# Performance work log

Hardware: AMD Instinct MI355X
Metric: run time of the kernel (lower is better)

The kernel has to match this reference:

```python
import jax, jax.numpy as jnp
import numpy as np

MARGIN_1 = 1.0
MARGIN_2 = 1.5
ALPHA_1 = 2.4
ALPHA_2 = 2.2
TVAL = 1.0
EPS = 1e-5


def setup_inputs() -> dict:
    key = jax.random.key(0)
    k1, k2, k3 = jax.random.split(key, 3)
    N, D = 4096, 2048
    x = jax.random.normal(k1, (N, D), dtype=jnp.float32)
    targets = jax.random.randint(k2, (N,), 0, 128, dtype=jnp.int32)
    sub = jax.random.randint(k3, (N,), 0, 2, dtype=jnp.int32)
    return {"x": x, "targets": targets, "sub": sub}


def _euclidean_dist(x):
    # pairwise distances of rows, clamped like torch .clamp(min=1e-12).sqrt()
    sq = jnp.sum(x * x, axis=1)  # [N]
    d2 = sq[:, None] + sq[None, :] - 2.0 * (x @ x.T)
    return jnp.sqrt(jnp.maximum(d2, 1e-12))  # [N, N]


def reference(x, targets, sub):
    # L2 normalize rows (norm=True path)
    x = x / jnp.maximum(jnp.linalg.norm(x, axis=1, keepdims=True), 1e-12)
    dist = _euclidean_dist(x)  # [N, N]
    N = dist.shape[0]

    eye = jnp.eye(N, dtype=bool)
    same_id = targets[:, None] == targets[None, :]
    is_pos = same_id & ~eye
    is_neg = ~same_id
    intra = sub[:, None] == sub[None, :]

    m_pos_intra = is_pos & intra
    m_pos_cross = is_pos & ~intra
    m_neg_intra = is_neg & intra
    m_neg_cross = is_neg & ~intra

    def ap_term(mask, margin, alpha):
        vals = jnp.maximum(dist + (margin - alpha), 0.0)
        cnt = jnp.sum(mask, axis=1).astype(dist.dtype)
        return jnp.sum(jnp.where(mask, vals, 0.0), axis=1) / (cnt + EPS)

    def an_term(mask, alpha):
        sel = mask & (dist < alpha)
        diff = alpha - dist  # = (alpha - d); weight = exp(tval * diff)
        w = jnp.where(sel, jnp.exp(TVAL * diff), 0.0)
        num = jnp.sum(jnp.where(sel, diff, 0.0) * w, axis=1)
        den = jnp.sum(w, axis=1) + EPS
        return num / den

    loss_rows = (
        ap_term(m_pos_intra, MARGIN_1, ALPHA_1)
        + ap_term(m_pos_cross, MARGIN_2, ALPHA_2)
        + an_term(m_neg_intra, ALPHA_1)
        + an_term(m_neg_cross, ALPHA_2)
    )
    return jnp.sum(loss_rows) / N
```

## Files before the change

### kernel.cpp

```cpp
#include <hip/hip_runtime.h>
#include <math.h>

#define THREADS 256
#define BM 128
#define QBK 128
#define EPSV 1e-5f
#define C1E 11.023176380641601f
#define C2E 9.025013499434122f
#define FP8_SCALE 256.0f
#define INV_SCALE2 1.52587890625e-5f

typedef float f32x4 __attribute__((ext_vector_type(4)));

__launch_bounds__(THREADS)
__global__ void norm_conv_fp8_kernel(const float* __restrict__ x,
                                     unsigned char* __restrict__ xq, int D) {
    const int row = blockIdx.x;
    const float4* x4 = (const float4*)(x + (size_t)row * D);
    const int tid = threadIdx.x;

    float s = 0.f;
    for (int b = tid * 2; b * 4 < D; b += THREADS * 2) {
        float4 v0 = x4[b];
        float4 v1 = x4[b + 1];
        s += v0.x * v0.x + v0.y * v0.y + v0.z * v0.z + v0.w * v0.w
           + v1.x * v1.x + v1.y * v1.y + v1.z * v1.z + v1.w * v1.w;
    }
#pragma unroll
    for (int off = 32; off > 0; off >>= 1) s += __shfl_down(s, off, 64);
    __shared__ float red[THREADS / 64 + 1];
    if ((tid & 63) == 0) red[tid >> 6] = s;
    __syncthreads();
    if (tid == 0) {
        float tot = 0.f;
#pragma unroll
        for (int w = 0; w < THREADS / 64; ++w) tot += red[w];
        red[THREADS / 64] = FP8_SCALE / fmaxf(sqrtf(tot), 1e-12f);
    }
    __syncthreads();
    const float sc = red[THREADS / 64];

    int2* out = (int2*)(xq + (size_t)row * D);
    for (int b = tid * 2; b * 4 < D; b += THREADS * 2) {
        float4 v0 = x4[b];
        float4 v1 = x4[b + 1];
        int lo = __builtin_amdgcn_cvt_pk_fp8_f32(v0.x * sc, v0.y * sc, 0, 0);
        lo = __builtin_amdgcn_cvt_pk_fp8_f32(v0.z * sc, v0.w * sc, lo, 1);
        int hi = __builtin_amdgcn_cvt_pk_fp8_f32(v1.x * sc, v1.y * sc, 0, 0);
        hi = __builtin_amdgcn_cvt_pk_fp8_f32(v1.z * sc, v1.w * sc, hi, 1);
        int2 o; o.x = lo; o.y = hi;
        out[b >> 1] = o;
    }
}

__global__ void row_inv_norm_kernel(const float* __restrict__ x,
                                    float* __restrict__ inv_norm, int D) {
    const int row = blockIdx.x;
    const float4* x4 = (const float4*)(x + (size_t)row * D);
    const int nf4 = D >> 2;
    float s = 0.f;
    for (int i = threadIdx.x; i < nf4; i += THREADS) {
        float4 v = x4[i];
        s += v.x * v.x + v.y * v.y + v.z * v.z + v.w * v.w;
    }
#pragma unroll
    for (int off = 32; off > 0; off >>= 1) s += __shfl_down(s, off, 64);
    __shared__ float red[THREADS / 64];
    if ((threadIdx.x & 63) == 0) red[threadIdx.x >> 6] = s;
    __syncthreads();
    if (threadIdx.x == 0) {
        float tot = 0.f;
#pragma unroll
        for (int w = 0; w < THREADS / 64; ++w) tot += red[w];
        inv_norm[row] = 1.0f / fmaxf(sqrtf(tot), 1e-12f);
    }
}

#define GLDS16(g, l)                                                          \
    __builtin_amdgcn_global_load_lds(                                         \
        (const __attribute__((address_space(1))) unsigned int*)(g),           \
        (__attribute__((address_space(3))) unsigned int*)(l), 16, 0, 0)

__launch_bounds__(THREADS, 2)
__global__ void gram_fp8_kernel(const unsigned char* __restrict__ xq,
                                const int* __restrict__ targets,
                                const int* __restrict__ sub,
                                float* __restrict__ pr,
                                float* __restrict__ pc,
                                int D) {
    __shared__ unsigned char As[2][BM * QBK];
    __shared__ unsigned char Bs[2][BM * QBK];

    const int tk = blockIdx.x;
    int bx = (int)((sqrtf(8.0f * tk + 1.0f) - 1.0f) * 0.5f);
    while ((bx + 1) * (bx + 2) / 2 <= tk) ++bx;
    while (bx * (bx + 1) / 2 > tk) --bx;
    const int by = tk - bx * (bx + 1) / 2;

    const int tid = threadIdx.x;
    const int w = tid >> 6;
    const int lane = tid & 63;
    const int wm = w & 1;
    const int wn = w >> 1;
    const int quad = lane >> 4;
    const int cl = lane & 15;

    const int rowA0 = by * BM;
    const int colB0 = bx * BM;
    const unsigned char* Abase = xq + (size_t)rowA0 * D;
    const unsigned char* Bbase = xq + (size_t)colB0 * D;

    const unsigned char* sA[4];
    const unsigned char* sB[4];
    int dof[4];
#pragma unroll
    for (int l = 0; l < 4; ++l) {
        const int c = l * 256 + tid;
        const int r = c >> 3, q = (c & 7) ^ ((c >> 3) & 7);
        sA[l] = Abase + (size_t)r * D + q * 16;
        sB[l] = Bbase + (size_t)r * D + q * 16;
        dof[l] = (l * 256 + w * 64) * 16;
    }

    f32x4 accv[4][4];
#pragma unroll
    for (int i = 0; i < 4; ++i)
#pragma unroll
        for (int j = 0; j < 4; ++j) accv[i][j] = (f32x4)(0.f);

    int aoff[4][4], boff[4][4];
#pragma unroll
    for (int f = 0; f < 4; ++f) {
        const int ar = wm * 64 + f * 16 + cl;
        const int br = wn * 64 + f * 16 + cl;
#pragma unroll
        for (int ks = 0; ks < 4; ++ks) {
            const int sl = ks * 4 + quad;
            aoff[f][ks] = ar * QBK + (((sl >> 1) ^ (ar & 7)) << 4)
                        + ((sl & 1) << 3);
            boff[f][ks] = br * QBK + (((sl >> 1) ^ (br & 7)) << 4)
                        + ((sl & 1) << 3);
        }
    }

    const int nIter = D / QBK;

#pragma unroll
    for (int l = 0; l < 4; ++l) {
        GLDS16(sA[l], &As[0][0] + dof[l]);
        GLDS16(sB[l], &Bs[0][0] + dof[l]);
    }
    __syncthreads();

    for (int it = 0; it < nIter; ++it) {
        const int cur = it & 1;
        const int nxt = cur ^ 1;

        if (it + 1 < nIter) {
            const int kb = (it + 1) * QBK;
#pragma unroll
            for (int l = 0; l < 4; ++l) {
                GLDS16(sA[l] + kb, &As[nxt][0] + dof[l]);
                GLDS16(sB[l] + kb, &Bs[nxt][0] + dof[l]);
            }
        }

#pragma unroll
        for (int ks = 0; ks < 4; ++ks) {
            long af[4], bfv[4];
#pragma unroll
            for (int f = 0; f < 4; ++f) {
                af[f] = *(const long*)&As[cur][aoff[f][ks]];
                bfv[f] = *(const long*)&Bs[cur][boff[f][ks]];
            }
#pragma unroll
            for (int mi = 0; mi < 4; ++mi)
#pragma unroll
                for (int ni = 0; ni < 4; ++ni)
                    accv[mi][ni] =
                        __builtin_amdgcn_mfma_f32_16x16x32_fp8_fp8(
                            af[mi], bfv[ni], accv[mi][ni], 0, 0, 0);
        }
        __syncthreads();
    }

    int tj[4], sj[4];
#pragma unroll
    for (int ni = 0; ni < 4; ++ni) {
        const int gc = colB0 + wn * 64 + ni * 16 + cl;
        tj[ni] = targets[gc];
        sj[ni] = sub[gc];
    }

#pragma unroll
    for (int mi = 0; mi < 4; ++mi) {
#pragma unroll
        for (int r = 0; r < 4; ++r) {
            const int gi = rowA0 + wm * 64 + mi * 16 + quad * 4 + r;
            const int ti = targets[gi];
            const int si = sub[gi];

            float s0 = 0.f, s1 = 0.f, s2 = 0.f, s3 = 0.f;
            float s4 = 0.f, s5 = 0.f, s6 = 0.f, s7 = 0.f;
#pragma unroll
            for (int ni = 0; ni < 4; ++ni) {
                const int gj = colB0 + wn * 64 + ni * 16 + cl;
                const float d2 =
                    fmaf(-2.0f * INV_SCALE2, accv[mi][ni][r], 2.0f);
                const float dd = sqrtf(fmaxf(d2, 1e-12f));
                accv[mi][ni][r] = dd;
                const bool same = (ti == tj[ni]);
                const bool intra = (si == sj[ni]);
                const bool pos = same && (gi != gj);
                const bool neg = !same;
                const float mg = intra ? 1.4f : 0.7f;
                const float v = fmaxf(dd - mg, 0.f);
                const float e = __expf(-dd);
                const float de = dd * e;
                if (pos && intra)  { s0 += v;  s1 += 1.f; }
                if (pos && !intra) { s2 += v;  s3 += 1.f; }
                if (neg && intra)  { s4 += de; s5 += e; }
                if (neg && !intra) { s6 += de; s7 += e; }
            }
#pragma unroll
            for (int off = 1; off < 16; off <<= 1) {
                s0 += __shfl_xor(s0, off, 64);
                s1 += __shfl_xor(s1, off, 64);
                s2 += __shfl_xor(s2, off, 64);
                s3 += __shfl_xor(s3, off, 64);
                s4 += __shfl_xor(s4, off, 64);
                s5 += __shfl_xor(s5, off, 64);
                s6 += __shfl_xor(s6, off, 64);
                s7 += __shfl_xor(s7, off, 64);
            }
            if (cl == 0) {
                const int rloc = wm * 64 + mi * 16 + quad * 4 + r;
                float* dst = pr +
                    ((size_t)(blockIdx.x * 2 + wn) * 128 + rloc) * 8;
                float4 p0 = {s0, s1, s2, s3};
                float4 p1 = {s4, s5, s6, s7};
                *(float4*)(dst) = p0;
                *(float4*)(dst + 4) = p1;
            }
        }
    }

    const float om = (bx == by) ? 0.f : 1.f;
#pragma unroll
    for (int ni = 0; ni < 4; ++ni) {
        const int gj = colB0 + wn * 64 + ni * 16 + cl;
        const int tjc = tj[ni];
        const int sjc = sj[ni];
        float s0 = 0.f, s1 = 0.f, s2 = 0.f, s3 = 0.f;
        float s4 = 0.f, s5 = 0.f, s6 = 0.f, s7 = 0.f;
#pragma unroll
        for (int mi = 0; mi < 4; ++mi) {
#pragma unroll
            for (int r = 0; r < 4; ++r) {
                const int gi = rowA0 + wm * 64 + mi * 16 + quad * 4 + r;
                const int ti = targets[gi];
                const int si = sub[gi];
                const float dd = accv[mi][ni][r];
                const bool same = (ti == tjc);
                const bool intra = (si == sjc);
                const bool pos = same && (gi != gj);
                const bool neg = !same;
                const float mg = intra ? 1.4f : 0.7f;
                const float v = fmaxf(dd - mg, 0.f);
                const float e = __expf(-dd);
                const float de = dd * e;
                if (pos && intra)  { s0 += v;  s1 += 1.f; }
                if (pos && !intra) { s2 += v;  s3 += 1.f; }
                if (neg && intra)  { s4 += de; s5 += e; }
                if (neg && !intra) { s6 += de; s7 += e; }
            }
        }
        s0 += __shfl_xor(s0, 16, 64); s0 += __shfl_xor(s0, 32, 64);
        s1 += __shfl_xor(s1, 16, 64); s1 += __shfl_xor(s1, 32, 64);
        s2 += __shfl_xor(s2, 16, 64); s2 += __shfl_xor(s2, 32, 64);
        s3 += __shfl_xor(s3, 16, 64); s3 += __shfl_xor(s3, 32, 64);
        s4 += __shfl_xor(s4, 16, 64); s4 += __shfl_xor(s4, 32, 64);
        s5 += __shfl_xor(s5, 16, 64); s5 += __shfl_xor(s5, 32, 64);
        s6 += __shfl_xor(s6, 16, 64); s6 += __shfl_xor(s6, 32, 64);
        s7 += __shfl_xor(s7, 16, 64); s7 += __shfl_xor(s7, 32, 64);
        if (lane < 16) {
            const int colloc = wn * 64 + ni * 16 + lane;
            float* dst = pc +
                ((size_t)(blockIdx.x * 2 + wm) * 128 + colloc) * 8;
            float4 p0 = {s0 * om, s1 * om, s2 * om, s3 * om};
            float4 p1 = {s4 * om, s5 * om, s6 * om, s7 * om};
            *(float4*)(dst) = p0;
            *(float4*)(dst + 4) = p1;
        }
    }
}

__global__ void finalize_sym_kernel(const float* __restrict__ pr,
                                    const float* __restrict__ pc,
                                    float* __restrict__ out, int N, int nbx) {
    const int tid = threadIdx.x;
    const int rloc16 = tid >> 4;
    const int st = tid & 15;
    const int i = blockIdx.x * 16 + rloc16;
    const int B = i >> 7;
    const int rl = i & 127;
    const int nrow = (nbx - B) * 2;

    float a0 = 0.f, a1 = 0.f, a2 = 0.f, a3 = 0.f;
    float a4 = 0.f, a5 = 0.f, a6 = 0.f, a7 = 0.f;
#pragma unroll
    for (int s4i = 0; s4i < 4; ++s4i) {
        const int sidx = st * 4 + s4i;
        const float* base;
        if (sidx < nrow) {
            const int bxx = B + (sidx >> 1);
            const int t = bxx * (bxx + 1) / 2 + B;
            base = pr + ((size_t)(t * 2 + (sidx & 1)) * 128 + rl) * 8;
        } else {
            const int m = sidx - nrow;
            const int t = B * (B + 1) / 2 + (m >> 1);
            base = pc + ((size_t)(t * 2 + (m & 1)) * 128 + rl) * 8;
        }
        float4 u0 = *(const float4*)(base);
        float4 u1 = *(const float4*)(base + 4);
        a0 += u0.x; a1 += u0.y; a2 += u0.z; a3 += u0.w;
        a4 += u1.x; a5 += u1.y; a6 += u1.z; a7 += u1.w;
    }
#pragma unroll
    for (int off = 1; off < 16; off <<= 1) {
        a0 += __shfl_xor(a0, off, 64);
        a1 += __shfl_xor(a1, off, 64);
        a2 += __shfl_xor(a2, off, 64);
        a3 += __shfl_xor(a3, off, 64);
        a4 += __shfl_xor(a4, off, 64);
        a5 += __shfl_xor(a5, off, 64);
        a6 += __shfl_xor(a6, off, 64);
        a7 += __shfl_xor(a7, off, 64);
    }
    __shared__ float lred[16];
    if (st == 0) {
        const float l = a0 / (a1 + EPSV) + a2 / (a3 + EPSV)
            + (C1E * fmaf(2.4f, a5, -a4)) / (C1E * a5 + EPSV)
            + (C2E * fmaf(2.2f, a7, -a6)) / (C2E * a7 + EPSV);
        lred[rloc16] = l;
    }
    __syncthreads();
    if (tid == 0) {
        float tot = 0.f;
#pragma unroll
        for (int k2 = 0; k2 < 16; ++k2) tot += lred[k2];
        atomicAdd(out, tot / (float)N);
    }
}

__launch_bounds__(THREADS, 2)
__global__ void dist_loss_kernel(const float* __restrict__ x,
                                 const int* __restrict__ targets,
                                 const int* __restrict__ sub,
                                 const float* __restrict__ inv_norm,
                                 float* __restrict__ acc,
                                 int N, int D) {
    __shared__ float Asf[16][128];
    __shared__ float Bsf[16][128];

    const int nbx = N / 128;
    const int bx = blockIdx.x % nbx;
    const int by = blockIdx.x / nbx;
    const int tid = threadIdx.x;
    const int tx = tid & 15;
    const int ty = tid >> 4;
    const int rowA0 = by * 128;
    const int colB0 = bx * 128;
    const float* Abase = x + (size_t)rowA0 * D;
    const float* Bbase = x + (size_t)colB0 * D;

    float accv[8][8];
#pragma unroll
    for (int r = 0; r < 8; ++r)
#pragma unroll
        for (int c = 0; c < 8; ++c) accv[r][c] = 0.f;

    for (int kb = 0; kb < D; kb += 16) {
#pragma unroll
        for (int l = 0; l < 2; ++l) {
            const int f = tid + l * THREADS;
            const int row = f >> 2;
            const int kq = (f & 3) << 2;
            float4 va = *(const float4*)(Abase + (size_t)row * D + kb + kq);
            float4 vb = *(const float4*)(Bbase + (size_t)row * D + kb + kq);
            Asf[kq + 0][row] = va.x; Asf[kq + 1][row] = va.y;
            Asf[kq + 2][row] = va.z; Asf[kq + 3][row] = va.w;
            Bsf[kq + 0][row] = vb.x; Bsf[kq + 1][row] = vb.y;
            Bsf[kq + 2][row] = vb.z; Bsf[kq + 3][row] = vb.w;
        }
        __syncthreads();
#pragma unroll
        for (int k = 0; k < 16; ++k) {
            float4 a0 = *(const float4*)&Asf[k][ty * 8];
            float4 a1 = *(const float4*)&Asf[k][ty * 8 + 4];
            float4 b0 = *(const float4*)&Bsf[k][tx * 8];
            float4 b1 = *(const float4*)&Bsf[k][tx * 8 + 4];
            float ar[8] = {a0.x, a0.y, a0.z, a0.w, a1.x, a1.y, a1.z, a1.w};
            float br[8] = {b0.x, b0.y, b0.z, b0.w, b1.x, b1.y, b1.z, b1.w};
#pragma unroll
            for (int r = 0; r < 8; ++r)
#pragma unroll
                for (int c = 0; c < 8; ++c)
                    accv[r][c] = fmaf(ar[r], br[c], accv[r][c]);
        }
        __syncthreads();
    }

    const int row_base = rowA0 + ty * 8;
    const int col_base = colB0 + tx * 8;
    int tjc[8], sjc[8];
    float invj[8];
#pragma unroll
    for (int c = 0; c < 8; ++c) {
        tjc[c] = targets[col_base + c];
        sjc[c] = sub[col_base + c];
        invj[c] = inv_norm[col_base + c];
    }
#pragma unroll
    for (int r = 0; r < 8; ++r) {
        const int gi = row_base + r;
        const int ti = targets[gi];
        const int si = sub[gi];
        const float invi = inv_norm[gi];
        float s0 = 0.f, s1 = 0.f, s2 = 0.f, s3 = 0.f;
        float s4 = 0.f, s5 = 0.f, s6 = 0.f, s7 = 0.f;
#pragma unroll
        for (int c = 0; c < 8; ++c) {
            const int gj = col_base + c;
            const float dot = accv[r][c] * invi * invj[c];
            const float dd = sqrtf(fmaxf(2.f - 2.f * dot, 1e-12f));
            const bool same = (ti == tjc[c]);
            const bool intra = (si == sjc[c]);
            const bool pos = same && (gi != gj);
            const bool neg = !same;
            const float df = (intra ? 2.4f : 2.2f) - dd;
            const float wgt = __expf(df);
            const float v = fmaxf(dd - (intra ? 1.4f : 0.7f), 0.f);
            if (pos && intra)  { s0 += v; s1 += 1.f; }
            if (pos && !intra) { s2 += v; s3 += 1.f; }
            if (neg && intra)  { s4 += df * wgt; s5 += wgt; }
            if (neg && !intra) { s6 += df * wgt; s7 += wgt; }
        }
#pragma unroll
        for (int off = 1; off < 16; off <<= 1) {
            s0 += __shfl_xor(s0, off, 64);
            s1 += __shfl_xor(s1, off, 64);
            s2 += __shfl_xor(s2, off, 64);
            s3 += __shfl_xor(s3, off, 64);
            s4 += __shfl_xor(s4, off, 64);
            s5 += __shfl_xor(s5, off, 64);
            s6 += __shfl_xor(s6, off, 64);
            s7 += __shfl_xor(s7, off, 64);
        }
        if (tx == 0) {
            float* a = acc + (size_t)gi * 8;
            atomicAdd(a + 0, s0); atomicAdd(a + 1, s1);
            atomicAdd(a + 2, s2); atomicAdd(a + 3, s3);
            atomicAdd(a + 4, s4); atomicAdd(a + 5, s5);
            atomicAdd(a + 6, s6); atomicAdd(a + 7, s7);
        }
    }
}

__global__ void finalize_kernel(const float* __restrict__ acc,
                                float* __restrict__ out, int N) {
    float s = 0.f;
    for (int i = threadIdx.x; i < N; i += THREADS) {
        const float* a = acc + (size_t)i * 8;
        s += a[0] / (a[1] + EPSV) + a[2] / (a[3] + EPSV)
           + a[4] / (a[5] + EPSV) + a[6] / (a[7] + EPSV);
    }
#pragma unroll
    for (int off = 32; off > 0; off >>= 1) s += __shfl_down(s, off, 64);
    __shared__ float red[THREADS / 64];
    if ((threadIdx.x & 63) == 0) red[threadIdx.x >> 6] = s;
    __syncthreads();
    if (threadIdx.x == 0) {
        float tot = 0.f;
#pragma unroll
        for (int w = 0; w < THREADS / 64; ++w) tot += red[w];
        out[0] = tot / (float)N;
    }
}

extern "C" void kernel_launch(void* const* d_in, const int* in_sizes, int n_in,
                              void* d_out, int out_size, void* d_ws, size_t ws_size,
                              hipStream_t stream) {
    const float* x = (const float*)d_in[0];
    const int* targets = (const int*)d_in[1];
    const int* sub = (const int*)d_in[2];
    const int N = in_sizes[1];
    const int D = in_sizes[0] / N;

    const int nbx = N / BM;
    const int T = nbx * (nbx + 1) / 2;
    const size_t sliceB = (size_t)T * 2 * 128 * 8 * sizeof(float);
    const size_t need = (size_t)N * D + 2 * sliceB;

    if (ws_size >= need) {
        unsigned char* xq = (unsigned char*)d_ws;
        float* pr = (float*)((char*)d_ws + (size_t)N * D);
        float* pc = pr + (size_t)T * 2 * 128 * 8;

        hipMemsetAsync(d_out, 0, sizeof(float), stream);
        norm_conv_fp8_kernel<<<N, THREADS, 0, stream>>>(x, xq, D);
        gram_fp8_kernel<<<T, THREADS, 0, stream>>>(xq, targets, sub,
                                                   pr, pc, D);
        finalize_sym_kernel<<<N / 16, THREADS, 0, stream>>>(
            pr, pc, (float*)d_out, N, nbx);
    } else {
        float* inv_norm = (float*)d_ws;
        float* acc = inv_norm + N;
        hipMemsetAsync(acc, 0, (size_t)N * 8 * sizeof(float), stream);
        row_inv_norm_kernel<<<N, THREADS, 0, stream>>>(x, inv_norm, D);
        dist_loss_kernel<<<nbx * nbx, THREADS, 0, stream>>>(
            x, targets, sub, inv_norm, acc, N, D);
        finalize_kernel<<<1, THREADS, 0, stream>>>(acc, (float*)d_out, N);
    }
}
```

Measured before the change: 163.0 us.

## Use 512-thread gram blocks with smaller K tile, LDS partial reduction, XCD remap

```diff
diff --git a/kernel.cpp b/kernel.cpp
--- a/kernel.cpp
+++ b/kernel.cpp
@@ -2,8 +2,9 @@
 #include <math.h>
 
 #define THREADS 256
+#define GT 512
 #define BM 128
-#define QBK 128
+#define QBK 64
 #define EPSV 1e-5f
 #define C1E 11.023176380641601f
 #define C2E 9.025013499434122f
@@ -81,7 +82,7 @@
         (const __attribute__((address_space(1))) unsigned int*)(g),           \
         (__attribute__((address_space(3))) unsigned int*)(l), 16, 0, 0)
 
-__launch_bounds__(THREADS, 2)
+__launch_bounds__(GT, 6)
 __global__ void gram_fp8_kernel(const unsigned char* __restrict__ xq,
                                 const int* __restrict__ targets,
                                 const int* __restrict__ sub,
@@ -91,7 +92,12 @@
     __shared__ unsigned char As[2][BM * QBK];
     __shared__ unsigned char Bs[2][BM * QBK];
 
-    const int tk = blockIdx.x;
+    int tk = blockIdx.x;
+    if ((gridDim.x & 7) == 0) {
+        const int per = gridDim.x >> 3;
+        tk = (tk & 7) * per + (tk >> 3);
+    }
+
     int bx = (int)((sqrtf(8.0f * tk + 1.0f) - 1.0f) * 0.5f);
     while ((bx + 1) * (bx + 2) / 2 <= tk) ++bx;
     while (bx * (bx + 1) / 2 > tk) --bx;
@@ -100,56 +106,44 @@
     const int tid = threadIdx.x;
     const int w = tid >> 6;
     const int lane = tid & 63;
-    const int wm = w & 1;
-    const int wn = w >> 1;
+    const int wm = w >> 2;
+    const int wn = w & 3;
     const int quad = lane >> 4;
     const int cl = lane & 15;
 
     const int rowA0 = by * BM;
     const int colB0 = bx * BM;
-    const unsigned char* Abase = xq + (size_t)rowA0 * D;
-    const unsigned char* Bbase = xq + (size_t)colB0 * D;
-
-    const unsigned char* sA[4];
-    const unsigned char* sB[4];
-    int dof[4];
-#pragma unroll
-    for (int l = 0; l < 4; ++l) {
-        const int c = l * 256 + tid;
-        const int r = c >> 3, q = (c & 7) ^ ((c >> 3) & 7);
-        sA[l] = Abase + (size_t)r * D + q * 16;
-        sB[l] = Bbase + (size_t)r * D + q * 16;
-        dof[l] = (l * 256 + w * 64) * 16;
-    }
-
-    f32x4 accv[4][4];
-#pragma unroll
-    for (int i = 0; i < 4; ++i)
-#pragma unroll
-        for (int j = 0; j < 4; ++j) accv[i][j] = (f32x4)(0.f);
-
-    int aoff[4][4], boff[4][4];
-#pragma unroll
-    for (int f = 0; f < 4; ++f) {
-        const int ar = wm * 64 + f * 16 + cl;
-        const int br = wn * 64 + f * 16 + cl;
-#pragma unroll
-        for (int ks = 0; ks < 4; ++ks) {
-            const int sl = ks * 4 + quad;
-            aoff[f][ks] = ar * QBK + (((sl >> 1) ^ (ar & 7)) << 4)
-                        + ((sl & 1) << 3);
-            boff[f][ks] = br * QBK + (((sl >> 1) ^ (br & 7)) << 4)
-                        + ((sl & 1) << 3);
-        }
-    }
+
+    const int r0 = tid >> 2;
+    const int qs = (tid & 3) ^ ((tid >> 3) & 3);
+    const unsigned char* sA = xq + (size_t)(rowA0 + r0) * D + qs * 16;
+    const unsigned char* sB = xq + (size_t)(colB0 + r0) * D + qs * 16;
+    const int dof = w * 1024;
+
+    int aoff[4], boff[2];
+#pragma unroll
+    for (int mi = 0; mi < 4; ++mi) {
+        const int ar = wm * 64 + mi * 16 + cl;
+        aoff[mi] = ar * QBK + ((((quad >> 1) ^ ((ar >> 1) & 3)) << 4))
+                 + ((quad & 1) << 3);
+    }
+#pragma unroll
+    for (int ni = 0; ni < 2; ++ni) {
+        const int br = wn * 32 + ni * 16 + cl;
+        boff[ni] = br * QBK + ((((quad >> 1) ^ ((br >> 1) & 3)) << 4))
+                 + ((quad & 1) << 3);
+    }
+
+    f32x4 accv[4][2];
+#pragma unroll
+    for (int mi = 0; mi < 4; ++mi)
+#pragma unroll
+        for (int ni = 0; ni < 2; ++ni) accv[mi][ni] = (f32x4)(0.f);
 
     const int nIter = D / QBK;
 
-#pragma unroll
-    for (int l = 0; l < 4; ++l) {
-        GLDS16(sA[l], &As[0][0] + dof[l]);
-        GLDS16(sB[l], &Bs[0][0] + dof[l]);
-    }
+    GLDS16(sA, &As[0][0] + dof);
+    GLDS16(sB, &Bs[0][0] + dof);
     __syncthreads();
 
     for (int it = 0; it < nIter; ++it) {
@@ -158,53 +152,62 @@
 
         if (it + 1 < nIter) {
             const int kb = (it + 1) * QBK;
-#pragma unroll
-            for (int l = 0; l < 4; ++l) {
-                GLDS16(sA[l] + kb, &As[nxt][0] + dof[l]);
-                GLDS16(sB[l] + kb, &Bs[nxt][0] + dof[l]);
-            }
-        }
-
-#pragma unroll
-        for (int ks = 0; ks < 4; ++ks) {
-            long af[4], bfv[4];
-#pragma unroll
-            for (int f = 0; f < 4; ++f) {
-                af[f] = *(const long*)&As[cur][aoff[f][ks]];
-                bfv[f] = *(const long*)&Bs[cur][boff[f][ks]];
-            }
-#pragma unroll
-            for (int mi = 0; mi < 4; ++mi)
-#pragma unroll
-                for (int ni = 0; ni < 4; ++ni)
-                    accv[mi][ni] =
-                        __builtin_amdgcn_mfma_f32_16x16x32_fp8_fp8(
-                            af[mi], bfv[ni], accv[mi][ni], 0, 0, 0);
-        }
+            GLDS16(sA + kb, &As[nxt][0] + dof);
+            GLDS16(sB + kb, &Bs[nxt][0] + dof);
+        }
+
+        long af[4], bfv[2];
+#pragma unroll
+        for (int mi = 0; mi < 4; ++mi)
+            af[mi] = *(const long*)&As[cur][aoff[mi]];
+#pragma unroll
+        for (int ni = 0; ni < 2; ++ni)
+            bfv[ni] = *(const long*)&Bs[cur][boff[ni]];
+#pragma unroll
+        for (int mi = 0; mi < 4; ++mi)
+#pragma unroll
+            for (int ni = 0; ni < 2; ++ni)
+                accv[mi][ni] = __builtin_amdgcn_mfma_f32_16x16x32_fp8_fp8(
+                    af[mi], bfv[ni], accv[mi][ni], 0, 0, 0);
+#pragma unroll
+        for (int mi = 0; mi < 4; ++mi)
+            af[mi] = *(const long*)&As[cur][aoff[mi] ^ 32];
+#pragma unroll
+        for (int ni = 0; ni < 2; ++ni)
+            bfv[ni] = *(const long*)&Bs[cur][boff[ni] ^ 32];
+#pragma unroll
+        for (int mi = 0; mi < 4; ++mi)
+#pragma unroll
+            for (int ni = 0; ni < 2; ++ni)
+                accv[mi][ni] = __builtin_amdgcn_mfma_f32_16x16x32_fp8_fp8(
+                    af[mi], bfv[ni], accv[mi][ni], 0, 0, 0);
+
         __syncthreads();
     }
 
-    int tj[4], sj[4];
-#pragma unroll
-    for (int ni = 0; ni < 4; ++ni) {
-        const int gc = colB0 + wn * 64 + ni * 16 + cl;
+    int tj[2], sj[2];
+#pragma unroll
+    for (int ni = 0; ni < 2; ++ni) {
+        const int gc = colB0 + wn * 32 + ni * 16 + cl;
         tj[ni] = targets[gc];
         sj[ni] = sub[gc];
     }
 
+    float* rowp = (float*)&As[0][0];
 #pragma unroll
     for (int mi = 0; mi < 4; ++mi) {
 #pragma unroll
         for (int r = 0; r < 4; ++r) {
-            const int gi = rowA0 + wm * 64 + mi * 16 + quad * 4 + r;
+            const int rloc = wm * 64 + mi * 16 + quad * 4 + r;
+            const int gi = rowA0 + rloc;
             const int ti = targets[gi];
             const int si = sub[gi];
 
             float s0 = 0.f, s1 = 0.f, s2 = 0.f, s3 = 0.f;
             float s4 = 0.f, s5 = 0.f, s6 = 0.f, s7 = 0.f;
 #pragma unroll
-            for (int ni = 0; ni < 4; ++ni) {
-                const int gj = colB0 + wn * 64 + ni * 16 + cl;
+            for (int ni = 0; ni < 2; ++ni) {
+                const int gj = colB0 + wn * 32 + ni * 16 + cl;
                 const float d2 =
                     fmaf(-2.0f * INV_SCALE2, accv[mi][ni][r], 2.0f);
                 const float dd = sqrtf(fmaxf(d2, 1e-12f));
@@ -234,9 +237,7 @@
                 s7 += __shfl_xor(s7, off, 64);
             }
             if (cl == 0) {
-                const int rloc = wm * 64 + mi * 16 + quad * 4 + r;
-                float* dst = pr +
-                    ((size_t)(blockIdx.x * 2 + wn) * 128 + rloc) * 8;
+                float* dst = rowp + ((wn << 7) + rloc) * 8;
                 float4 p0 = {s0, s1, s2, s3};
                 float4 p1 = {s4, s5, s6, s7};
                 *(float4*)(dst) = p0;
@@ -244,11 +245,18 @@
             }
         }
     }
-
-    const float om = (bx == by) ? 0.f : 1.f;
-#pragma unroll
-    for (int ni = 0; ni < 4; ++ni) {
-        const int gj = colB0 + wn * 64 + ni * 16 + cl;
+    __syncthreads();
+    {
+        const size_t prbase = (size_t)tk * 1024;
+        for (int i = tid; i < 1024; i += GT)
+            pr[prbase + i] = rowp[i] + rowp[1024 + i]
+                           + rowp[2048 + i] + rowp[3072 + i];
+    }
+
+    float* colp = (float*)&Bs[0][0];
+#pragma unroll
+    for (int ni = 0; ni < 2; ++ni) {
+        const int gj = colB0 + wn * 32 + ni * 16 + cl;
         const int tjc = tj[ni];
         const int sjc = sj[ni];
         float s0 = 0.f, s1 = 0.f, s2 = 0.f, s3 = 0.f;
@@ -284,14 +292,20 @@
         s6 += __shfl_xor(s6, 16, 64); s6 += __shfl_xor(s6, 32, 64);
         s7 += __shfl_xor(s7, 16, 64); s7 += __shfl_xor(s7, 32, 64);
         if (lane < 16) {
-            const int colloc = wn * 64 + ni * 16 + lane;
-            float* dst = pc +
-                ((size_t)(blockIdx.x * 2 + wm) * 128 + colloc) * 8;
-            float4 p0 = {s0 * om, s1 * om, s2 * om, s3 * om};
-            float4 p1 = {s4 * om, s5 * om, s6 * om, s7 * om};
+            const int colloc = wn * 32 + ni * 16 + lane;
+            float* dst = colp + ((wm << 7) + colloc) * 8;
+            float4 p0 = {s0, s1, s2, s3};
+            float4 p1 = {s4, s5, s6, s7};
             *(float4*)(dst) = p0;
             *(float4*)(dst + 4) = p1;
         }
+    }
+    __syncthreads();
+    {
+        const float om = (bx == by) ? 0.f : 1.f;
+        const size_t pcbase = (size_t)tk * 1024;
+        for (int i = tid; i < 1024; i += GT)
+            pc[pcbase + i] = (colp[i] + colp[1024 + i]) * om;
     }
 }
 
@@ -304,22 +318,19 @@
     const int i = blockIdx.x * 16 + rloc16;
     const int B = i >> 7;
     const int rl = i & 127;
-    const int nrow = (nbx - B) * 2;
+    const int nrow = nbx - B;
+    const int ntot = nbx + 1;
 
     float a0 = 0.f, a1 = 0.f, a2 = 0.f, a3 = 0.f;
     float a4 = 0.f, a5 = 0.f, a6 = 0.f, a7 = 0.f;
-#pragma unroll
-    for (int s4i = 0; s4i < 4; ++s4i) {
-        const int sidx = st * 4 + s4i;
+    for (int s = st; s < ntot; s += 16) {
         const float* base;
-        if (sidx < nrow) {
-            const int bxx = B + (sidx >> 1);
-            const int t = bxx * (bxx + 1) / 2 + B;
-            base = pr + ((size_t)(t * 2 + (sidx & 1)) * 128 + rl) * 8;
+        if (s < nrow) {
+            const int bxx = B + s;
+            base = pr + ((size_t)(bxx * (bxx + 1) / 2 + B) * 128 + rl) * 8;
         } else {
-            const int m = sidx - nrow;
-            const int t = B * (B + 1) / 2 + (m >> 1);
-            base = pc + ((size_t)(t * 2 + (m & 1)) * 128 + rl) * 8;
+            const int byy = s - nrow;
+            base = pc + ((size_t)(B * (B + 1) / 2 + byy) * 128 + rl) * 8;
         }
         float4 u0 = *(const float4*)(base);
         float4 u1 = *(const float4*)(base + 4);
@@ -499,18 +510,17 @@
 
     const int nbx = N / BM;
     const int T = nbx * (nbx + 1) / 2;
-    const size_t sliceB = (size_t)T * 2 * 128 * 8 * sizeof(float);
+    const size_t sliceB = (size_t)T * 128 * 8 * sizeof(float);
     const size_t need = (size_t)N * D + 2 * sliceB;
 
     if (ws_size >= need) {
         unsigned char* xq = (unsigned char*)d_ws;
         float* pr = (float*)((char*)d_ws + (size_t)N * D);
-        float* pc = pr + (size_t)T * 2 * 128 * 8;
+        float* pc = pr + (size_t)T * 128 * 8;
 
         hipMemsetAsync(d_out, 0, sizeof(float), stream);
         norm_conv_fp8_kernel<<<N, THREADS, 0, stream>>>(x, xq, D);
-        gram_fp8_kernel<<<T, THREADS, 0, stream>>>(xq, targets, sub,
-                                                   pr, pc, D);
+        gram_fp8_kernel<<<T, GT, 0, stream>>>(xq, targets, sub, pr, pc, D);
         finalize_sym_kernel<<<N / 16, THREADS, 0, stream>>>(
             pr, pc, (float*)d_out, N, nbx);
     } else {
```

Measured after the change: 179.7 us. 10.3% more time.
